# Optimization experiments

Measured on AMD Instinct MI355X. Metric: run time of the kernel, lower is better.

Reference implementation:

```python
import jax, jax.numpy as jnp
import numpy as np

B, T, DM = 4, 2048, 1024
H, DK, DV = 16, 64, 64


def setup_inputs() -> dict:
    key = jax.random.key(0)
    k1, k2, k3, k4 = jax.random.split(key, 4)
    x = jax.random.normal(k1, (B, T, DM), dtype=jnp.float32)
    scale = 0.02
    Wq = jax.random.normal(k2, (H, DM, DK), dtype=jnp.float32) * scale
    Wk = jax.random.normal(k3, (H, DM, DK), dtype=jnp.float32) * scale
    Wv = jax.random.normal(k4, (H, DM, DV), dtype=jnp.float32) * scale
    return {"x": x, "Wq": Wq, "Wk": Wk, "Wv": Wv}


def reference(x, Wq, Wk, Wv):
    # Per-head projections, vectorized over heads: [B,H,T,dk]
    q = jnp.einsum('btd,hdk->bhtk', x, Wq)
    k = jnp.einsum('btd,hdk->bhtk', x, Wk)
    v = jnp.einsum('btd,hdv->bhtv', x, Wv)
    scale = DK ** -0.5  # k.shape[-1] ** -0.5 in original
    wei = jnp.einsum('bhtk,bhsk->bhts', q, k) * scale  # [B,H,T,T]
    causal = jnp.tril(jnp.ones((T, T), dtype=bool))
    wei = jnp.where(causal, wei, -jnp.inf)
    wei = jax.nn.softmax(wei, axis=-1)
    # dropout p=0.0 -> identity (eval-mode equivalent)
    out = jnp.einsum('bhts,bhsv->bhtv', wei, v)  # [B,H,T,dv]
    # concat heads along last dim: [B,T,H*dv]
    return out.transpose(0, 2, 1, 3).reshape(B, T, H * DV)
```

## Files before the change

### kernel.cpp

```cpp
#include <hip/hip_runtime.h>


#define B_  4
#define T_  2048
#define DM_ 1024
#define H_  16
#define D_  64
#define DMO 1024

typedef unsigned short u16;
typedef unsigned int   u32;
typedef u16   u16x8  __attribute__((ext_vector_type(8)));
typedef short s16x8  __attribute__((ext_vector_type(8)));
typedef float f32x4  __attribute__((ext_vector_type(4)));
typedef float f32x16 __attribute__((ext_vector_type(16)));
typedef u32   u32x2  __attribute__((ext_vector_type(2)));
typedef u32   u32x4  __attribute__((ext_vector_type(4)));

#if __has_builtin(__builtin_amdgcn_exp2f)
#define EXP2(x) __builtin_amdgcn_exp2f(x)
#else
#define EXP2(x) __expf((x) * 0.69314718f)
#endif

#define WAIT_BAR(N) do {                                                      \
    asm volatile("s_waitcnt vmcnt(" #N ")" ::: "memory");                     \
    __builtin_amdgcn_s_barrier();                                             \
    __builtin_amdgcn_sched_barrier(0); } while (0)
#define BAR_ONLY() do {                                                       \
    __builtin_amdgcn_s_barrier();                                             \
    __builtin_amdgcn_sched_barrier(0); } while (0)

__device__ __forceinline__ u16 f2bf_hu(float f) {
    u32 u = __builtin_bit_cast(u32, f) + 0x8000u;
    return (u16)(u >> 16);
}
__device__ __forceinline__ u32 pk2(float lo, float hi) {
    u32 ul = __builtin_bit_cast(u32, lo) + 0x8000u;
    u32 uh = __builtin_bit_cast(u32, hi) + 0x8000u;
    return __builtin_amdgcn_perm(uh, ul, 0x07060302);
}
__device__ __forceinline__ u16x8 cvt8(const float* s) {
    f32x4 a = *(const f32x4*)s;
    f32x4 b = *(const f32x4*)(s + 4);
    u32x4 r { pk2(a[0], a[1]), pk2(a[2], a[3]), pk2(b[0], b[1]), pk2(b[2], b[3]) };
    return __builtin_bit_cast(u16x8, r);
}
__device__ __forceinline__ f32x4 mfma16(u16x8 a, u16x8 b, f32x4 c) {
    return __builtin_amdgcn_mfma_f32_16x16x32_bf16(
        __builtin_bit_cast(s16x8, a), __builtin_bit_cast(s16x8, b), c, 0, 0, 0);
}
__device__ __forceinline__ f32x16 mfma32(u16x8 a, u16x8 b, f32x16 c) {
    return __builtin_amdgcn_mfma_f32_32x32x16_bf16(
        __builtin_bit_cast(s16x8, a), __builtin_bit_cast(s16x8, b), c, 0, 0, 0);
}
__device__ __forceinline__ void gld_lds16(const u16* g, u16* l) {
    __builtin_amdgcn_global_load_lds(
        (const __attribute__((address_space(1))) u32*)g,
        (__attribute__((address_space(3))) u32*)l, 16, 0, 0);
}

__global__ __launch_bounds__(256) void cvt_all(
    const float* __restrict__ x,  const float* __restrict__ Wq,
    const float* __restrict__ Wk, const float* __restrict__ Wv,
    u16* __restrict__ xb, u16* __restrict__ Wt)
{
    __shared__ u16 L[64][74];
    const int bx = blockIdx.x;
    if (bx < 1024) {
        size_t i0 = ((size_t)bx * 256 + threadIdx.x) * 32;
        #pragma unroll
        for (int c = 0; c < 4; c++)
            *(u16x8*)(xb + i0 + c * 8) = cvt8(x + i0 + c * 8);
        return;
    }
    const int wb = bx - 1024;
    const int dblk = wb & 15, h = (wb >> 4) & 15, mat = wb >> 8;
    const float* W = (mat == 0) ? Wq : (mat == 1) ? Wk : Wv;
    const int tid = threadIdx.x;
    {
        const int dl = tid >> 2, c = (tid & 3) * 16;
        const float* src = W + ((size_t)h * DM_ + dblk * 64 + dl) * D_ + c;
        #pragma unroll
        for (int g = 0; g < 2; g++)
            *(u16x8*)&L[dl][c + g * 8] = cvt8(src + g * 8);
    }
    __syncthreads();
    {
        const int dkr = tid >> 2, g = tid & 3;
        u16 tmp[16];
        #pragma unroll
        for (int j = 0; j < 16; j++) tmp[j] = L[g * 16 + j][dkr];
        u16* dst = Wt + ((size_t)(mat * 16 + h) * 64 + dkr) * DM_ + dblk * 64 + g * 16;
        *(u16x8*)dst = *(u16x8*)tmp;
        *(u16x8*)(dst + 8) = *(u16x8*)(tmp + 8);
    }
}

template<int SWAP>
__device__ __forceinline__ void pcompute(const char* Asb, const char* Bsb,
                                         int wm, int wn, int quad, int l16,
                                         int ax, f32x4 (&acc)[4][4]) {
    #pragma unroll
    for (int ks = 0; ks < 2; ks++) {
        u16x8 af[4], bf[4];
        #pragma unroll
        for (int i = 0; i < 4; i++)
            af[i] = *(const u16x8*)(Asb +
                ((((wm * 64 + i * 16 + l16) * 64 + ks * 32 + quad * 8) * 2) ^ ax));
        #pragma unroll
        for (int j = 0; j < 4; j++)
            bf[j] = *(const u16x8*)(Bsb +
                ((((wn * 64 + j * 16 + l16) * 64 + ks * 32 + quad * 8) * 2) ^ ax));
        __builtin_amdgcn_s_setprio(1);
        #pragma unroll
        for (int i = 0; i < 4; i++)
            #pragma unroll
            for (int j = 0; j < 4; j++)
                acc[i][j] = SWAP ? mfma16(bf[j], af[i], acc[i][j])
                                 : mfma16(af[i], bf[j], acc[i][j]);
        __builtin_amdgcn_s_setprio(0);
    }
}

__global__ __launch_bounds__(256) void proj_kernel(
    const u16* __restrict__ xb, const u16* __restrict__ Wt,
    u16* __restrict__ Qc, u16* __restrict__ Kc, u16* __restrict__ Vtc)
{
    __shared__ __attribute__((aligned(16))) u16 As0[128][64];
    __shared__ __attribute__((aligned(16))) u16 Bs0[128][64];
    __shared__ __attribute__((aligned(16))) u16 As1[128][64];
    __shared__ __attribute__((aligned(16))) u16 Bs1[128][64];

    const int pb = blockIdx.x;
    const int mt = (pb & 7) * 8 + ((pb >> 3) & 7);
    const int nti = pb >> 6;
    const int m0 = mt * 128;
    const int n0 = nti * 128;
    const int mat = n0 >> 10;
    const int tid  = threadIdx.x;
    const int wave = tid >> 6, lane = tid & 63;
    const int quad = lane >> 4, l16 = lane & 15;
    const int wm   = wave >> 1, wn = wave & 1;

    const int r8 = lane >> 3, g8 = lane & 7;
    const int gs = (g8 ^ r8) * 8;
    const int ax = (l16 & 7) << 4;

    f32x4 acc[4][4];
    #pragma unroll
    for (int i = 0; i < 4; i++)
        #pragma unroll
        for (int j = 0; j < 4; j++) acc[i][j] = f32x4{0.f, 0.f, 0.f, 0.f};

    auto STAGE = [&](u16* Ad, u16* Bd, int kb) {
        const int kbase = kb * 64;
        #pragma unroll
        for (int it = 0; it < 4; it++) {
            const int row = it * 32 + wave * 8 + r8;
            const int ldo = (it * 4 + wave) * 512 + lane * 8;
            gld_lds16(xb + (size_t)(m0 + row) * DM_ + kbase + gs, Ad + ldo);
            gld_lds16(Wt + (size_t)(n0 + row) * DM_ + kbase + gs, Bd + ldo);
        }
    };

    STAGE(&As0[0][0], &Bs0[0][0], 0);
    STAGE(&As1[0][0], &Bs1[0][0], 1);

    #define PLOOP(SW)                                                        \
        for (int j = 0; j < 8; j++) {                                        \
            WAIT_BAR(8);                                                     \
            pcompute<SW>((const char*)As0, (const char*)Bs0,                 \
                         wm, wn, quad, l16, ax, acc);                        \
            BAR_ONLY();                                                      \
            if (2 * j + 2 < 16) STAGE(&As0[0][0], &Bs0[0][0], 2 * j + 2);    \
            if (j < 7) { WAIT_BAR(8); } else { WAIT_BAR(0); }                \
            pcompute<SW>((const char*)As1, (const char*)Bs1,                 \
                         wm, wn, quad, l16, ax, acc);                        \
            BAR_ONLY();                                                      \
            if (2 * j + 3 < 16) STAGE(&As1[0][0], &Bs1[0][0], 2 * j + 3);    \
        }
    if (mat != 2) { PLOOP(1) } else { PLOOP(0) }
    #undef PLOOP

    const int h_base = (n0 & 1023) >> 6;
    if (mat != 2) {
        u16* Cm = (mat == 0) ? Qc : Kc;
        const float sc = (mat == 0) ? 0.18033688f : 1.0f;
        #pragma unroll
        for (int i = 0; i < 4; i++) {
            const int m  = m0 + wm * 64 + i * 16 + l16;
            const int bb = m >> 11, t = m & (T_ - 1);
            u16* rowp = Cm + ((size_t)(bb * H_ + h_base + wn) * T_ + t) * D_;
            #pragma unroll
            for (int j = 0; j < 4; j++) {
                const int dk0 = j * 16 + quad * 4;
                u32x2 d { pk2(acc[i][j][0] * sc, acc[i][j][1] * sc),
                          pk2(acc[i][j][2] * sc, acc[i][j][3] * sc) };
                *(u32x2*)(rowp + dk0) = d;
            }
        }
    } else {
        #pragma unroll
        for (int i = 0; i < 4; i++) {
            const int m  = m0 + wm * 64 + i * 16 + quad * 4;
            const int bb = m >> 11, t = m & (T_ - 1);
            #pragma unroll
            for (int j = 0; j < 4; j++) {
                const int dk = j * 16 + l16;
                u32x2 d { pk2(acc[i][j][0], acc[i][j][1]),
                          pk2(acc[i][j][2], acc[i][j][3]) };
                *(u32x2*)(Vtc + ((size_t)(bb * H_ + h_base + wn) * D_ + dk) * T_ + t) = d;
            }
        }
    }
}

__global__ __launch_bounds__(512, 2) void attn_kernel(
    const u16* __restrict__ Qc, const u16* __restrict__ Kc,
    const u16* __restrict__ Vtc, float* __restrict__ out)
{
    __shared__ __attribute__((aligned(16))) u16 Ks0[64][64];
    __shared__ __attribute__((aligned(16))) u16 Vs0[64][64];
    __shared__ __attribute__((aligned(16))) u16 Ks1[64][64];
    __shared__ __attribute__((aligned(16))) u16 Vs1[64][64];

    const int pb  = blockIdx.x;
    const int bh  = (pb & 7) * 8 + ((pb >> 3) & 7);
    const int g   = 7 - (pb >> 6);
    const int h   = bh & 15, b = bh >> 4;

    const int tid = threadIdx.x, w = tid >> 6, lane = tid & 63;
    const int l31 = lane & 31, hi = lane >> 5;
    const int r8 = (tid >> 3) & 7, g8 = tid & 7;
    const int gs = (g8 ^ r8) * 8;
    const int ax = (l31 & 7) << 4;

    const int qrow = g * 256 + w * 32 + l31;
    const int i_d  = g * 4 + (w >> 1);
    const int nt   = g * 4 + 4;
    const int qmask = 32 * (w & 1) + l31;

    const u16* Qbh = Qc + (size_t)(b * H_ + h) * T_ * D_;
    const u16* Kbh = Kc + (size_t)(b * H_ + h) * T_ * D_;
    const u16* Vbh = Vtc + (size_t)(b * H_ + h) * D_ * T_;

    auto STAGE = [&](u16* Kd, u16* Vd, int t) {
        const int sbase = t * 64;
        const int row = tid >> 3;
        const int ldo = tid * 8;
        gld_lds16(Kbh + (size_t)(sbase + row) * D_ + gs, Kd + ldo);
        gld_lds16(Vbh + (size_t)row * T_ + sbase + gs,  Vd + ldo);
    };

    u16x8 qf[4];
    #pragma unroll
    for (int ks = 0; ks < 4; ks++)
        qf[ks] = *(const u16x8*)(Qbh + (size_t)qrow * D_ + ks * 16 + hi * 8);

    f32x16 zz;
    #pragma unroll
    for (int r = 0; r < 16; r++) zz[r] = 0.f;

    f32x16 ot0, ot1;
    #pragma unroll
    for (int r = 0; r < 16; r++) { ot0[r] = 0.f; ot1[r] = 0.f; }
    float mi = -1e30f, li = 0.f;

    auto COMPUTE = [&](const char* Ksb, const char* Vsb, int i) {
        f32x16 st0, st1;
        __builtin_amdgcn_s_setprio(1);
        {
            const int co = (hi * 8) * 2;
            u16x8 k0 = *(const u16x8*)(Ksb + ((l31 * 128 + co) ^ ax));
            u16x8 k1 = *(const u16x8*)(Ksb + (((32 + l31) * 128 + co) ^ ax));
            st0 = mfma32(k0, qf[0], zz);
            st1 = mfma32(k1, qf[0], zz);
        }
        #pragma unroll
        for (int ks = 1; ks < 4; ks++) {
            const int co = (ks * 16 + hi * 8) * 2;
            u16x8 k0 = *(const u16x8*)(Ksb + ((l31 * 128 + co) ^ ax));
            u16x8 k1 = *(const u16x8*)(Ksb + (((32 + l31) * 128 + co) ^ ax));
            st0 = mfma32(k0, qf[ks], st0);
            st1 = mfma32(k1, qf[ks], st1);
        }
        __builtin_amdgcn_s_setprio(0);

        if (i == i_d) {
            #pragma unroll
            for (int r = 0; r < 16; r++) {
                const int sl = (r & 3) + 8 * (r >> 2) + 4 * hi;
                if (sl > qmask)      st0[r] = -1e30f;
                if (sl + 32 > qmask) st1[r] = -1e30f;
            }
        }

        float mx = -1e30f;
        #pragma unroll
        for (int r = 0; r < 16; r++) mx = fmaxf(mx, fmaxf(st0[r], st1[r]));
        mx = fmaxf(mx, __shfl_xor(mx, 32));
        if (!__all(mx - mi <= 8.f)) {
            const float mn = fmaxf(mi, mx);
            const float al = EXP2(mi - mn);
            li *= al;
            #pragma unroll
            for (int r = 0; r < 16; r++) { ot0[r] *= al; ot1[r] *= al; }
            mi = mn;
        }
        float sum = 0.f;
        #pragma unroll
        for (int r = 0; r < 16; r++) {
            const float p0 = EXP2(st0[r] - mi);
            const float p1 = EXP2(st1[r] - mi);
            st0[r] = p0; st1[r] = p1;
            sum += p0 + p1;
        }
        sum += __shfl_xor(sum, 32);
        li += sum;

        u16x8 pb4[4];
        #define PACK(SRC, C, OUT) {                                           \
            u32 d0 = pk2(SRC[8*(C)+0], SRC[8*(C)+1]);                         \
            u32 d1 = pk2(SRC[8*(C)+2], SRC[8*(C)+3]);                         \
            u32 d2 = pk2(SRC[8*(C)+4], SRC[8*(C)+5]);                         \
            u32 d3 = pk2(SRC[8*(C)+6], SRC[8*(C)+7]);                         \
            u32 e0 = __shfl_xor(hi ? d0 : d2, 32);                            \
            u32 e1 = __shfl_xor(hi ? d1 : d3, 32);                            \
            u32x4 wds{ hi ? e0 : d0, hi ? e1 : d1,                            \
                       hi ? d2 : e0, hi ? d3 : e1 };                          \
            OUT = __builtin_bit_cast(u16x8, wds); }
        PACK(st0, 0, pb4[0]); PACK(st0, 1, pb4[1]);
        PACK(st1, 0, pb4[2]); PACK(st1, 1, pb4[3]);
        #undef PACK

        __builtin_amdgcn_s_setprio(1);
        #pragma unroll
        for (int kc = 0; kc < 4; kc++) {
            const int co = (kc * 16 + hi * 8) * 2;
            u16x8 v0 = *(const u16x8*)(Vsb + ((l31 * 128 + co) ^ ax));
            u16x8 v1 = *(const u16x8*)(Vsb + (((32 + l31) * 128 + co) ^ ax));
            ot0 = mfma32(v0, pb4[kc], ot0);
            ot1 = mfma32(v1, pb4[kc], ot1);
        }
        __builtin_amdgcn_s_setprio(0);
    };

    STAGE(&Ks0[0][0], &Vs0[0][0], 0);
    STAGE(&Ks1[0][0], &Vs1[0][0], 1);

    const int np = nt >> 1;
    for (int j = 0; j < np; j++) {
        const int i0 = 2 * j, i1 = 2 * j + 1;
        WAIT_BAR(2);
        if (i0 <= i_d) COMPUTE((const char*)Ks0, (const char*)Vs0, i0);
        BAR_ONLY();
        if (i0 + 2 < nt) STAGE(&Ks0[0][0], &Vs0[0][0], i0 + 2);
        if (j < np - 1) { WAIT_BAR(2); } else { WAIT_BAR(0); }
        if (i1 <= i_d) COMPUTE((const char*)Ks1, (const char*)Vs1, i1);
        BAR_ONLY();
        if (i1 + 2 < nt) STAGE(&Ks1[0][0], &Vs1[0][0], i1 + 2);
    }

    const float inv = 1.0f / li;
    float* orow = out + (size_t)(b * T_ + qrow) * DMO + h * D_;
    #pragma unroll
    for (int c = 0; c < 2; c++)
        #pragma unroll
        for (int hf = 0; hf < 2; hf++) {
            f32x4 v0, v1;
            #pragma unroll
            for (int j = 0; j < 4; j++) {
                v0[j] = ot0[c * 8 + hf * 4 + j] * inv;
                v1[j] = ot1[c * 8 + hf * 4 + j] * inv;
            }
            *(f32x4*)(orow + c * 16 + hf * 8 + hi * 4)      = v0;
            *(f32x4*)(orow + 32 + c * 16 + hf * 8 + hi * 4) = v1;
        }
}

extern "C" void kernel_launch(void* const* d_in, const int* in_sizes, int n_in,
                              void* d_out, int out_size, void* d_ws, size_t ws_size,
                              hipStream_t stream) {
    int xi = 0, wi[3] = {1, 2, 3};
    {
        int k = 0, found = 0;
        for (int i = 0; i < n_in && i < 8; i++) {
            if (in_sizes[i] == B_ * T_ * DM_) { xi = i; found = 1; }
            else if (in_sizes[i] == H_ * DM_ * D_ && k < 3) wi[k++] = i;
        }
        if (!found || k != 3) { xi = 0; wi[0] = 1; wi[1] = 2; wi[2] = 3; }
    }
    const float* x  = (const float*)d_in[xi];
    const float* Wq = (const float*)d_in[wi[0]];
    const float* Wk = (const float*)d_in[wi[1]];
    const float* Wv = (const float*)d_in[wi[2]];
    float* out = (float*)d_out;

    u16* xb = (u16*)d_out;
    u16* Wt = xb + (size_t)B_ * T_ * DM_;
    const size_t per = (size_t)B_ * H_ * T_ * D_;
    u16* Qc  = (u16*)d_ws;
    u16* Kc  = Qc + per;
    u16* Vtc = Kc + per;

    cvt_all<<<1792, 256, 0, stream>>>(x, Wq, Wk, Wv, xb, Wt);
    proj_kernel<<<1536, 256, 0, stream>>>(xb, Wt, Qc, Kc, Vtc);
    attn_kernel<<<512, 512, 0, stream>>>(Qc, Kc, Vtc, out);
}
```

Baseline: 216.5 us.

## Use hardware bf16 pack, packed softmax math, and reorder causal tile scheduling

Replaces the software round-and-perm bf16 packing of attention probabilities with the v_cvt_pk_bf16_f32 instruction. Restructures the row max as a pairwise reduction and the exp/sum loop around two-wide float vectors so the compiler can emit packed subtract and add instructions. Changes block-to-query-group mapping so the second half of blocks runs groups in ascending order instead of descending, changing how causal work is spread across CUs. The hardware convert rounds differently from the old truncation-style add, which may slightly change numerics.

```diff
diff --git a/kernel.cpp b/kernel.cpp
--- a/kernel.cpp
+++ b/kernel.cpp
@@ -12,6 +12,7 @@
 typedef unsigned int   u32;
 typedef u16   u16x8  __attribute__((ext_vector_type(8)));
 typedef short s16x8  __attribute__((ext_vector_type(8)));
+typedef float f32x2  __attribute__((ext_vector_type(2)));
 typedef float f32x4  __attribute__((ext_vector_type(4)));
 typedef float f32x16 __attribute__((ext_vector_type(16)));
 typedef u32   u32x2  __attribute__((ext_vector_type(2)));
@@ -39,6 +40,11 @@
     u32 ul = __builtin_bit_cast(u32, lo) + 0x8000u;
     u32 uh = __builtin_bit_cast(u32, hi) + 0x8000u;
     return __builtin_amdgcn_perm(uh, ul, 0x07060302);
+}
+__device__ __forceinline__ u32 cvtpk(float lo, float hi) {
+    u32 r;
+    asm("v_cvt_pk_bf16_f32 %0, %1, %2" : "=v"(r) : "v"(lo), "v"(hi));
+    return r;
 }
 __device__ __forceinline__ u16x8 cvt8(const float* s) {
     f32x4 a = *(const f32x4*)s;
@@ -227,7 +233,7 @@
 
     const int pb  = blockIdx.x;
     const int bh  = (pb & 7) * 8 + ((pb >> 3) & 7);
-    const int g   = 7 - (pb >> 6);
+    const int g   = (pb < 256) ? (7 - (pb >> 6)) : ((pb - 256) >> 6);
     const int h   = bh & 15, b = bh >> 4;
 
     const int tid = threadIdx.x, w = tid >> 6, lane = tid & 63;
@@ -296,9 +302,11 @@
             }
         }
 
-        float mx = -1e30f;
-        #pragma unroll
-        for (int r = 0; r < 16; r++) mx = fmaxf(mx, fmaxf(st0[r], st1[r]));
+        float mx = fmaxf(st0[0], st0[1]);
+        #pragma unroll
+        for (int r = 2; r < 16; r += 2) mx = fmaxf(fmaxf(mx, st0[r]), st0[r + 1]);
+        #pragma unroll
+        for (int r = 0; r < 16; r += 2) mx = fmaxf(fmaxf(mx, st1[r]), st1[r + 1]);
         mx = fmaxf(mx, __shfl_xor(mx, 32));
         if (!__all(mx - mi <= 8.f)) {
             const float mn = fmaxf(mi, mx);
@@ -308,23 +316,30 @@
             for (int r = 0; r < 16; r++) { ot0[r] *= al; ot1[r] *= al; }
             mi = mn;
         }
-        float sum = 0.f;
-        #pragma unroll
-        for (int r = 0; r < 16; r++) {
-            const float p0 = EXP2(st0[r] - mi);
-            const float p1 = EXP2(st1[r] - mi);
-            st0[r] = p0; st1[r] = p1;
-            sum += p0 + p1;
-        }
+
+        f32x2 mm; mm[0] = mi; mm[1] = mi;
+        f32x2 sac; sac[0] = 0.f; sac[1] = 0.f;
+        #pragma unroll
+        for (int k = 0; k < 8; k++) {
+            f32x2 a; a[0] = st0[2 * k]; a[1] = st0[2 * k + 1];
+            f32x2 c; c[0] = st1[2 * k]; c[1] = st1[2 * k + 1];
+            a = a - mm; c = c - mm;
+            a[0] = EXP2(a[0]); a[1] = EXP2(a[1]);
+            c[0] = EXP2(c[0]); c[1] = EXP2(c[1]);
+            st0[2 * k] = a[0]; st0[2 * k + 1] = a[1];
+            st1[2 * k] = c[0]; st1[2 * k + 1] = c[1];
+            sac = sac + a; sac = sac + c;
+        }
+        float sum = sac[0] + sac[1];
         sum += __shfl_xor(sum, 32);
         li += sum;
 
         u16x8 pb4[4];
         #define PACK(SRC, C, OUT) {                                           \
-            u32 d0 = pk2(SRC[8*(C)+0], SRC[8*(C)+1]);                         \
-            u32 d1 = pk2(SRC[8*(C)+2], SRC[8*(C)+3]);                         \
-            u32 d2 = pk2(SRC[8*(C)+4], SRC[8*(C)+5]);                         \
-            u32 d3 = pk2(SRC[8*(C)+6], SRC[8*(C)+7]);                         \
+            u32 d0 = cvtpk(SRC[8*(C)+0], SRC[8*(C)+1]);                       \
+            u32 d1 = cvtpk(SRC[8*(C)+2], SRC[8*(C)+3]);                       \
+            u32 d2 = cvtpk(SRC[8*(C)+4], SRC[8*(C)+5]);                       \
+            u32 d3 = cvtpk(SRC[8*(C)+6], SRC[8*(C)+7]);                       \
             u32 e0 = __shfl_xor(hi ? d0 : d2, 32);                            \
             u32 e1 = __shfl_xor(hi ? d1 : d3, 32);                            \
             u32x4 wds{ hi ? e0 : d0, hi ? e1 : d1,                            \
```

Result: no change. 213.9 us (-1.2%).
